# Kernel tuning notes

Hardware: AMD Instinct MI355X
Metric: run time of the kernel (lower is better)

Reference implementation:

```python
import jax, jax.numpy as jnp
import numpy as np

E = 256            # embedding_dim
S = 16             # num_surv_samples
N = 8192           # batch of events
NUM_NODES = 20000  # max_dst_idx - min_src_idx + 1
N_SRC = 10000
MIN_DST = 10000
TD_HR_MAX = 5000.0


def setup_inputs() -> dict:
    key = jax.random.key(0)
    ks = jax.random.split(key, 16)
    all_embeddings = jax.random.normal(ks[0], (NUM_NODES, E), dtype=jnp.float32)
    assoc = jnp.arange(NUM_NODES, dtype=jnp.int64 if jax.config.jax_enable_x64 else jnp.int32)
    src = jax.random.randint(ks[1], (N,), 0, N_SRC)
    pos_dst = jax.random.randint(ks[2], (N,), 0, N_SRC) + MIN_DST
    last_update = jax.random.uniform(ks[3], (NUM_NODES,), dtype=jnp.float32) * 1000.0
    last_time_pos = jax.random.uniform(ks[4], (N,), dtype=jnp.float32) * 1000.0
    cur_time = 2000.0 + jax.random.uniform(ks[5], (N,), dtype=jnp.float32) * 100.0
    u_non_embeddings = jax.random.normal(ks[6], (S * N, E), dtype=jnp.float32)
    v_non_embeddings = jax.random.normal(ks[7], (S * N, E), dtype=jnp.float32)
    td_surv_step = jax.random.uniform(ks[8], (S, N), dtype=jnp.float32)
    event_inten_accu = jax.random.uniform(ks[9], (N_SRC, N_SRC), dtype=jnp.float32)
    W_omega = jax.random.normal(ks[10], (1, 2 * E), dtype=jnp.float32) * (1.0 / np.sqrt(2 * E))
    b_omega = jax.random.normal(ks[11], (1,), dtype=jnp.float32) * 0.01
    psi = 0.5 * jnp.ones((1,), dtype=jnp.float32)
    alpha = jax.random.uniform(ks[12], (1,), dtype=jnp.float32)
    w_t = jax.random.uniform(ks[13], (1,), dtype=jnp.float32)
    return dict(all_embeddings=all_embeddings, assoc=assoc, src=src, pos_dst=pos_dst,
                last_update=last_update, cur_time=cur_time,
                u_non_embeddings=u_non_embeddings, v_non_embeddings=v_non_embeddings,
                last_time_pos=last_time_pos, td_surv_step=td_surv_step,
                event_inten_accu=event_inten_accu, W_omega=W_omega, b_omega=b_omega,
                psi=psi, alpha=alpha, w_t=w_t)


def _hawkes_intensity(z_u, z_v, td, W, b, psi, alpha, w_t):
    # symmetric=False path of hawkes_intensity_singleType
    Wu, Wv = W[0, :E], W[0, E:]          # split Linear over [z_u; z_v] concat
    g = z_u @ Wu + z_v @ Wv + b[0]       # [M]
    td_norm = td / TD_HR_MAX
    g = g + alpha[0] * jnp.exp(-w_t[0] * td_norm)
    g_psi = jnp.clip(g / (psi[0] + 1e-7), -75.0, 75.0)
    return psi[0] * (jnp.log1p(jnp.exp(-g_psi)) + g_psi)


def reference(all_embeddings, assoc, src, pos_dst, last_update, cur_time,
              u_non_embeddings, v_non_embeddings, last_time_pos, td_surv_step,
              event_inten_accu, W_omega, b_omega, psi, alpha, w_t):
    z_src = all_embeddings[assoc[src]]
    z_dst = all_embeddings[assoc[pos_dst]]
    lu_src = last_update[assoc[src]]
    lu_dst = last_update[assoc[pos_dst]]

    td_pos = cur_time - last_time_pos  # (unused downstream on this branch)
    last_update_max = jnp.maximum(lu_src, lu_dst)
    use_accu = (last_time_pos >= last_update_max).astype(jnp.float32)
    t_uv = jnp.maximum(last_update_max, last_time_pos)
    td_uv = cur_time - t_uv

    # unit_sampling=False: Monte-Carlo survival samples
    td_uv_non = td_surv_step * td_uv[None, :]          # [S, N]

    lambda_uv = _hawkes_intensity(z_src, z_dst, td_uv, W_omega, b_omega, psi, alpha, w_t)
    lambda_surv = _hawkes_intensity(u_non_embeddings, v_non_embeddings,
                                    td_uv_non.reshape(-1), W_omega, b_omega,
                                    psi, alpha, w_t).reshape(S, N)

    integral = jnp.mean(lambda_surv, axis=0) * td_uv \
        + use_accu * event_inten_accu[src, pos_dst - MIN_DST]
    loss_surv = jnp.sum(integral)
    loss_lambda = -jnp.sum(jnp.log(lambda_uv + 1e-7))

    n = z_src.shape[0]
    return (loss_lambda / n, loss_surv / n)
```

## Files before the change

kernel.cpp:

```cpp
#include <hip/hip_runtime.h>

constexpr int   S_    = 16;
constexpr int   N_    = 8192;
constexpr int   NSRC  = 10000;
constexpr int   MINDST= 10000;
constexpr float TDMAX = 5000.0f;

__device__ __forceinline__ float wave_reduce_sum(float v) {
#pragma unroll
    for (int off = 32; off > 0; off >>= 1)
        v += __shfl_xor(v, off, 64);
    return v;
}

__device__ __forceinline__ float hawkes(float gdot, float td,
                                        float b, float psi, float alpha, float wt) {
    float g  = gdot + b + alpha * expf(-wt * (td * (1.0f / TDMAX)));
    float gp = g / (psi + 1e-7f);
    gp = fminf(fmaxf(gp, -75.0f), 75.0f);
    return psi * (log1pf(expf(-gp)) + gp);
}

__global__ __launch_bounds__(256) void decoder_tp_fused(
    const float* __restrict__ emb,
    const int*   __restrict__ assoc,
    const int*   __restrict__ src,
    const int*   __restrict__ dst,
    const float* __restrict__ last_update,
    const float* __restrict__ cur_time,
    const float* __restrict__ u_non,
    const float* __restrict__ v_non,
    const float* __restrict__ last_time_pos,
    const float* __restrict__ td_step,
    const float* __restrict__ accu,
    const float* __restrict__ W,
    const float* __restrict__ b_p,
    const float* __restrict__ psi_p,
    const float* __restrict__ alpha_p,
    const float* __restrict__ wt_p,
    float* __restrict__ out)
{
    const int wave = threadIdx.x >> 6;
    const int lane = threadIdx.x & 63;
    const int i    = (blockIdx.x << 2) + wave;

    const float4* __restrict__ W4 = (const float4*)W;
    const float4 wu = W4[lane];
    const float4 wv = W4[64 + lane];
    const float b0    = b_p[0];
    const float psi   = psi_p[0];
    const float alpha = alpha_p[0];
    const float wt    = wt_p[0];

    const int si = src[i];
    const int di = dst[i];
    const int as = assoc[si];
    const int ad = assoc[di];
    const float lum  = fmaxf(last_update[as], last_update[ad]);
    const float ltp  = last_time_pos[i];
    const float ct   = cur_time[i];
    const float t_uv = fmaxf(lum, ltp);
    const float td_uv = ct - t_uv;

    const float4* __restrict__ Z4 = (const float4*)emb;
    const float4 zs = Z4[(size_t)as * 64 + lane];
    const float4 zd = Z4[(size_t)ad * 64 + lane];
    float d = zs.x * wu.x + zs.y * wu.y + zs.z * wu.z + zs.w * wu.w
            + zd.x * wv.x + zd.y * wv.y + zd.z * wv.z + zd.w * wv.w;
    d = wave_reduce_sum(d);
    const float lam_uv = hawkes(d, td_uv, b0, psi, alpha, wt);
    const float loss_lambda = -logf(lam_uv + 1e-7f);

    const float4* __restrict__ U4 = (const float4*)u_non;
    const float4* __restrict__ V4 = (const float4*)v_non;
    float lam_sum = 0.0f;
#pragma unroll 4
    for (int s = 0; s < S_; ++s) {
        const size_t p = (size_t)s * N_ + i;
        const float4 uu = U4[p * 64 + lane];
        const float4 vv = V4[p * 64 + lane];
        float dd = uu.x * wu.x + uu.y * wu.y + uu.z * wu.z + uu.w * wu.w
                 + vv.x * wv.x + vv.y * wv.y + vv.z * wv.z + vv.w * wv.w;
        dd = wave_reduce_sum(dd);
        lam_sum += hawkes(dd, td_step[p] * td_uv, b0, psi, alpha, wt);
    }
    float loss_surv = lam_sum * (1.0f / S_) * td_uv;
    if (ltp >= lum)
        loss_surv += accu[(size_t)si * NSRC + (di - MINDST)];

    __shared__ float s_ll[4], s_sv[4];
    if (lane == 0) { s_ll[wave] = loss_lambda; s_sv[wave] = loss_surv; }
    __syncthreads();
    if (threadIdx.x == 0) {
        const float a = s_ll[0] + s_ll[1] + s_ll[2] + s_ll[3];
        const float c = s_sv[0] + s_sv[1] + s_sv[2] + s_sv[3];
        atomicAdd(&out[0], a * (1.0f / N_));
        atomicAdd(&out[1], c * (1.0f / N_));
    }
}

extern "C" void kernel_launch(void* const* d_in, const int* in_sizes, int n_in,
                              void* d_out, int out_size, void* d_ws, size_t ws_size,
                              hipStream_t stream) {
    const float* emb           = (const float*)d_in[0];
    const int*   assoc         = (const int*)  d_in[1];
    const int*   src           = (const int*)  d_in[2];
    const int*   dst           = (const int*)  d_in[3];
    const float* last_update   = (const float*)d_in[4];
    const float* cur_time      = (const float*)d_in[5];
    const float* u_non         = (const float*)d_in[6];
    const float* v_non         = (const float*)d_in[7];
    const float* last_time_pos = (const float*)d_in[8];
    const float* td_step       = (const float*)d_in[9];
    const float* accu          = (const float*)d_in[10];
    const float* W             = (const float*)d_in[11];
    const float* b_p           = (const float*)d_in[12];
    const float* psi_p         = (const float*)d_in[13];
    const float* alpha_p       = (const float*)d_in[14];
    const float* wt_p          = (const float*)d_in[15];
    float* out = (float*)d_out;

    hipMemsetAsync(out, 0, 2 * sizeof(float), stream);

    decoder_tp_fused<<<N_ / 4, 256, 0, stream>>>(
        emb, assoc, src, dst, last_update, cur_time, u_non, v_non,
        last_time_pos, td_step, accu, W, b_p, psi_p, alpha_p, wt_p, out);
}
```

Measured before the change: 638.1 us.

## Split fused decoder into per-sample survival, lambda, and finalize kernels

The survival Monte-Carlo part now runs as its own kernel with one wave per (sample, event) pair, giving 16x more blocks instead of looping over 16 samples inside each wave. This is meant to expose more memory-level parallelism on the large u/v streams, which make up most of the traffic. The lambda and accu gathers move to a separate kernel. Global atomics are replaced by per-block partial sums in workspace plus a single-block finalize kernel, which removes the memset and atomics but adds two launches and recomputes td_uv per sample.

New measurement: 655.4 us. 2.7% more time.

```diff
diff --git a/kernel.cpp b/kernel.cpp
--- a/kernel.cpp
+++ b/kernel.cpp
@@ -1,10 +1,13 @@
 #include <hip/hip_runtime.h>
 
-constexpr int   S_    = 16;
-constexpr int   N_    = 8192;
-constexpr int   NSRC  = 10000;
-constexpr int   MINDST= 10000;
-constexpr float TDMAX = 5000.0f;
+constexpr int   S_     = 16;
+constexpr int   N_     = 8192;
+constexpr int   NSRC   = 10000;
+constexpr int   MINDST = 10000;
+constexpr float TDMAX  = 5000.0f;
+
+constexpr int SURV_BLOCKS = (S_ * N_) / 4;
+constexpr int LAM_BLOCKS  = N_ / 4;
 
 __device__ __forceinline__ float wave_reduce_sum(float v) {
 #pragma unroll
@@ -21,24 +24,79 @@
     return psi * (log1pf(expf(-gp)) + gp);
 }
 
-__global__ __launch_bounds__(256) void decoder_tp_fused(
+__global__ __launch_bounds__(256) void surv_kernel(
+    const int*   __restrict__ src,
+    const int*   __restrict__ dst,
+    const int*   __restrict__ assoc,
+    const float* __restrict__ last_update,
+    const float* __restrict__ cur_time,
+    const float* __restrict__ last_time_pos,
+    const float* __restrict__ u_non,
+    const float* __restrict__ v_non,
+    const float* __restrict__ td_step,
+    const float* __restrict__ W,
+    const float* __restrict__ b_p,
+    const float* __restrict__ psi_p,
+    const float* __restrict__ alpha_p,
+    const float* __restrict__ wt_p,
+    float* __restrict__ ws_s)
+{
+    const int wave = threadIdx.x >> 6;
+    const int lane = threadIdx.x & 63;
+    const int q    = (blockIdx.x << 2) + wave;
+    const int i    = q & (N_ - 1);
+
+    const float4* __restrict__ W4 = (const float4*)W;
+    const float4 wu = W4[lane];
+    const float4 wv = W4[64 + lane];
+
+    const float4* __restrict__ U4 = (const float4*)u_non;
+    const float4* __restrict__ V4 = (const float4*)v_non;
+    const float4 uu = U4[(size_t)q * 64 + lane];
+    const float4 vv = V4[(size_t)q * 64 + lane];
+    const float ts = td_step[q];
+
+    const int si = src[i];
+    const int di = dst[i];
+    const int as = assoc[si];
+    const int ad = assoc[di];
+    const float lum   = fmaxf(last_update[as], last_update[ad]);
+    const float td_uv = cur_time[i] - fmaxf(lum, last_time_pos[i]);
+
+    float d = uu.x * wu.x + uu.y * wu.y + uu.z * wu.z + uu.w * wu.w
+            + vv.x * wv.x + vv.y * wv.y + vv.z * wv.z + vv.w * wv.w;
+    d = wave_reduce_sum(d);
+
+    const float b0    = b_p[0];
+    const float psi   = psi_p[0];
+    const float alpha = alpha_p[0];
+    const float wt    = wt_p[0];
+    const float contrib = hawkes(d, ts * td_uv, b0, psi, alpha, wt)
+                        * td_uv * (1.0f / S_);
+
+    __shared__ float sh[4];
+    if (lane == 0) sh[wave] = contrib;
+    __syncthreads();
+    if (threadIdx.x == 0)
+        ws_s[blockIdx.x] = sh[0] + sh[1] + sh[2] + sh[3];
+}
+
+__global__ __launch_bounds__(256) void lambda_kernel(
     const float* __restrict__ emb,
     const int*   __restrict__ assoc,
     const int*   __restrict__ src,
     const int*   __restrict__ dst,
     const float* __restrict__ last_update,
     const float* __restrict__ cur_time,
-    const float* __restrict__ u_non,
-    const float* __restrict__ v_non,
     const float* __restrict__ last_time_pos,
-    const float* __restrict__ td_step,
     const float* __restrict__ accu,
     const float* __restrict__ W,
     const float* __restrict__ b_p,
     const float* __restrict__ psi_p,
     const float* __restrict__ alpha_p,
     const float* __restrict__ wt_p,
-    float* __restrict__ out)
+    float* __restrict__ ws_l,
+    float* __restrict__ ws_a)
 {
     const int wave = threadIdx.x >> 6;
     const int lane = threadIdx.x & 63;
@@ -47,20 +105,16 @@
     const float4* __restrict__ W4 = (const float4*)W;
     const float4 wu = W4[lane];
     const float4 wv = W4[64 + lane];
-    const float b0    = b_p[0];
-    const float psi   = psi_p[0];
-    const float alpha = alpha_p[0];
-    const float wt    = wt_p[0];
 
     const int si = src[i];
     const int di = dst[i];
     const int as = assoc[si];
     const int ad = assoc[di];
-    const float lum  = fmaxf(last_update[as], last_update[ad]);
-    const float ltp  = last_time_pos[i];
-    const float ct   = cur_time[i];
-    const float t_uv = fmaxf(lum, ltp);
-    const float td_uv = ct - t_uv;
+    const float lus = last_update[as];
+    const float lud = last_update[ad];
+    const float lum = fmaxf(lus, lud);
+    const float ltp = last_time_pos[i];
+    const float td_uv = cur_time[i] - fmaxf(lum, ltp);
 
     const float4* __restrict__ Z4 = (const float4*)emb;
     const float4 zs = Z4[(size_t)as * 64 + lane];
@@ -68,34 +122,45 @@
     float d = zs.x * wu.x + zs.y * wu.y + zs.z * wu.z + zs.w * wu.w
             + zd.x * wv.x + zd.y * wv.y + zd.z * wv.z + zd.w * wv.w;
     d = wave_reduce_sum(d);
-    const float lam_uv = hawkes(d, td_uv, b0, psi, alpha, wt);
-    const float loss_lambda = -logf(lam_uv + 1e-7f);
-
-    const float4* __restrict__ U4 = (const float4*)u_non;
-    const float4* __restrict__ V4 = (const float4*)v_non;
-    float lam_sum = 0.0f;
-#pragma unroll 4
-    for (int s = 0; s < S_; ++s) {
-        const size_t p = (size_t)s * N_ + i;
-        const float4 uu = U4[p * 64 + lane];
-        const float4 vv = V4[p * 64 + lane];
-        float dd = uu.x * wu.x + uu.y * wu.y + uu.z * wu.z + uu.w * wu.w
-                 + vv.x * wv.x + vv.y * wv.y + vv.z * wv.z + vv.w * wv.w;
-        dd = wave_reduce_sum(dd);
-        lam_sum += hawkes(dd, td_step[p] * td_uv, b0, psi, alpha, wt);
-    }
-    float loss_surv = lam_sum * (1.0f / S_) * td_uv;
-    if (ltp >= lum)
-        loss_surv += accu[(size_t)si * NSRC + (di - MINDST)];
-
-    __shared__ float s_ll[4], s_sv[4];
-    if (lane == 0) { s_ll[wave] = loss_lambda; s_sv[wave] = loss_surv; }
+
+    const float lam = hawkes(d, td_uv, b_p[0], psi_p[0], alpha_p[0], wt_p[0]);
+    const float part_l = -logf(lam + 1e-7f);
+
+    float part_a = accu[(size_t)si * NSRC + (di - MINDST)];
+    part_a = (ltp >= lum) ? part_a : 0.0f;
+
+    __shared__ float shl[4], sha[4];
+    if (lane == 0) { shl[wave] = part_l; sha[wave] = part_a; }
     __syncthreads();
     if (threadIdx.x == 0) {
-        const float a = s_ll[0] + s_ll[1] + s_ll[2] + s_ll[3];
-        const float c = s_sv[0] + s_sv[1] + s_sv[2] + s_sv[3];
-        atomicAdd(&out[0], a * (1.0f / N_));
-        atomicAdd(&out[1], c * (1.0f / N_));
+        ws_l[blockIdx.x] = shl[0] + shl[1] + shl[2] + shl[3];
+        ws_a[blockIdx.x] = sha[0] + sha[1] + sha[2] + sha[3];
+    }
+}
+
+__global__ __launch_bounds__(256) void finalize_kernel(
+    const float* __restrict__ ws_s,
+    const float* __restrict__ ws_l,
+    const float* __restrict__ ws_a,
+    float* __restrict__ out)
+{
+    float sS = 0.0f, sL = 0.0f;
+    for (int j = threadIdx.x; j < SURV_BLOCKS; j += 256) sS += ws_s[j];
+    for (int j = threadIdx.x; j < LAM_BLOCKS; j += 256) {
+        sS += ws_a[j];
+        sL += ws_l[j];
+    }
+    sS = wave_reduce_sum(sS);
+    sL = wave_reduce_sum(sL);
+
+    __shared__ float shS[4], shL[4];
+    const int wave = threadIdx.x >> 6;
+    const int lane = threadIdx.x & 63;
+    if (lane == 0) { shS[wave] = sS; shL[wave] = sL; }
+    __syncthreads();
+    if (threadIdx.x == 0) {
+        out[0] = (shL[0] + shL[1] + shL[2] + shL[3]) * (1.0f / N_);
+        out[1] = (shS[0] + shS[1] + shS[2] + shS[3]) * (1.0f / N_);
     }
 }
 
@@ -120,9 +185,17 @@
     const float* wt_p          = (const float*)d_in[15];
     float* out = (float*)d_out;
 
-    hipMemsetAsync(out, 0, 2 * sizeof(float), stream);
-
-    decoder_tp_fused<<<N_ / 4, 256, 0, stream>>>(
-        emb, assoc, src, dst, last_update, cur_time, u_non, v_non,
-        last_time_pos, td_step, accu, W, b_p, psi_p, alpha_p, wt_p, out);
-}
+    float* ws_s = (float*)d_ws;
+    float* ws_l = ws_s + SURV_BLOCKS;
+    float* ws_a = ws_l + LAM_BLOCKS;
+
+    surv_kernel<<<SURV_BLOCKS, 256, 0, stream>>>(
+        src, dst, assoc, last_update, cur_time, last_time_pos,
+        u_non, v_non, td_step, W, b_p, psi_p, alpha_p, wt_p, ws_s);
+
+    lambda_kernel<<<LAM_BLOCKS, 256, 0, stream>>>(
+        emb, assoc, src, dst, last_update, cur_time, last_time_pos,
+        accu, W, b_p, psi_p, alpha_p, wt_p, ws_l, ws_a);
+
+    finalize_kernel<<<1, 256, 0, stream>>>(ws_s, ws_l, ws_a, out);
+}
```

## Spread survival samples across waves and replace atomics with two-stage reduction

Applied to the files above, without the earlier changes.

Each wave now handles two survival samples (u/v rows) instead of one event's sixteen, so the grid grows from 2048 to 16384 blocks and all sample loads are issued up front for more memory-level parallelism. The per-event data (src/dst, last_update, td_uv) is recomputed by each wave that needs it, while the positive-pair intensity and accu term are computed only by the first N waves. Per-block partial sums go to workspace and a single-block finalize kernel reduces them, replacing the global atomics and the memset. This trades redundant per-event index and gather work and an extra launch for higher occupancy and streaming bandwidth on the dominant u/v read.

New measurement: 645.0 us. No clear change (+1.1%).

```diff
diff --git a/kernel.cpp b/kernel.cpp
--- a/kernel.cpp
+++ b/kernel.cpp
@@ -1,10 +1,13 @@
 #include <hip/hip_runtime.h>
 
-constexpr int   S_    = 16;
-constexpr int   N_    = 8192;
-constexpr int   NSRC  = 10000;
-constexpr int   MINDST= 10000;
-constexpr float TDMAX = 5000.0f;
+constexpr int   S_     = 16;
+constexpr int   N_     = 8192;
+constexpr int   NSRC   = 10000;
+constexpr int   MINDST = 10000;
+constexpr float TDMAX  = 5000.0f;
+
+constexpr int TOTAL_WAVES = S_ * N_ / 2;
+constexpr int MAIN_BLOCKS = TOTAL_WAVES / 4;
 
 __device__ __forceinline__ float wave_reduce_sum(float v) {
 #pragma unroll
@@ -21,16 +24,16 @@
     return psi * (log1pf(expf(-gp)) + gp);
 }
 
-__global__ __launch_bounds__(256) void decoder_tp_fused(
+__global__ __launch_bounds__(256) void fused_kernel(
     const float* __restrict__ emb,
     const int*   __restrict__ assoc,
     const int*   __restrict__ src,
     const int*   __restrict__ dst,
     const float* __restrict__ last_update,
     const float* __restrict__ cur_time,
+    const float* __restrict__ last_time_pos,
     const float* __restrict__ u_non,
     const float* __restrict__ v_non,
-    const float* __restrict__ last_time_pos,
     const float* __restrict__ td_step,
     const float* __restrict__ accu,
     const float* __restrict__ W,
@@ -38,64 +41,97 @@
     const float* __restrict__ psi_p,
     const float* __restrict__ alpha_p,
     const float* __restrict__ wt_p,
-    float* __restrict__ out)
+    float* __restrict__ ws_s,
+    float* __restrict__ ws_l)
 {
     const int wave = threadIdx.x >> 6;
     const int lane = threadIdx.x & 63;
-    const int i    = (blockIdx.x << 2) + wave;
+    const int w    = (blockIdx.x << 2) + wave;
+    const int q0   = w;
+    const int q1   = w + TOTAL_WAVES;
+    const int i    = w & (N_ - 1);
+
+    const float4* __restrict__ U4 = (const float4*)u_non;
+    const float4* __restrict__ V4 = (const float4*)v_non;
+    const float4 u0 = U4[(size_t)q0 * 64 + lane];
+    const float4 v0 = V4[(size_t)q0 * 64 + lane];
+    const float4 u1 = U4[(size_t)q1 * 64 + lane];
+    const float4 v1 = V4[(size_t)q1 * 64 + lane];
+    const float ts0 = td_step[q0];
+    const float ts1 = td_step[q1];
 
     const float4* __restrict__ W4 = (const float4*)W;
     const float4 wu = W4[lane];
     const float4 wv = W4[64 + lane];
+
+    const int si = src[i];
+    const int di = dst[i];
+    const int as = assoc[si];
+    const int ad = assoc[di];
+    const float lum   = fmaxf(last_update[as], last_update[ad]);
+    const float ltp   = last_time_pos[i];
+    const float td_uv = cur_time[i] - fmaxf(lum, ltp);
+
     const float b0    = b_p[0];
     const float psi   = psi_p[0];
     const float alpha = alpha_p[0];
     const float wt    = wt_p[0];
 
-    const int si = src[i];
-    const int di = dst[i];
-    const int as = assoc[si];
-    const int ad = assoc[di];
-    const float lum  = fmaxf(last_update[as], last_update[ad]);
-    const float ltp  = last_time_pos[i];
-    const float ct   = cur_time[i];
-    const float t_uv = fmaxf(lum, ltp);
-    const float td_uv = ct - t_uv;
+    float d0 = u0.x * wu.x + u0.y * wu.y + u0.z * wu.z + u0.w * wu.w
+             + v0.x * wv.x + v0.y * wv.y + v0.z * wv.z + v0.w * wv.w;
+    float d1 = u1.x * wu.x + u1.y * wu.y + u1.z * wu.z + u1.w * wu.w
+             + v1.x * wv.x + v1.y * wv.y + v1.z * wv.z + v1.w * wv.w;
+    d0 = wave_reduce_sum(d0);
+    d1 = wave_reduce_sum(d1);
 
-    const float4* __restrict__ Z4 = (const float4*)emb;
-    const float4 zs = Z4[(size_t)as * 64 + lane];
-    const float4 zd = Z4[(size_t)ad * 64 + lane];
-    float d = zs.x * wu.x + zs.y * wu.y + zs.z * wu.z + zs.w * wu.w
-            + zd.x * wv.x + zd.y * wv.y + zd.z * wv.z + zd.w * wv.w;
-    d = wave_reduce_sum(d);
-    const float lam_uv = hawkes(d, td_uv, b0, psi, alpha, wt);
-    const float loss_lambda = -logf(lam_uv + 1e-7f);
+    float contrib = (hawkes(d0, ts0 * td_uv, b0, psi, alpha, wt) +
+                     hawkes(d1, ts1 * td_uv, b0, psi, alpha, wt))
+                  * td_uv * (1.0f / S_);
+    float part_l = 0.0f;
 
-    const float4* __restrict__ U4 = (const float4*)u_non;
-    const float4* __restrict__ V4 = (const float4*)v_non;
-    float lam_sum = 0.0f;
-#pragma unroll 4
-    for (int s = 0; s < S_; ++s) {
-        const size_t p = (size_t)s * N_ + i;
-        const float4 uu = U4[p * 64 + lane];
-        const float4 vv = V4[p * 64 + lane];
-        float dd = uu.x * wu.x + uu.y * wu.y + uu.z * wu.z + uu.w * wu.w
-                 + vv.x * wv.x + vv.y * wv.y + vv.z * wv.z + vv.w * wv.w;
-        dd = wave_reduce_sum(dd);
-        lam_sum += hawkes(dd, td_step[p] * td_uv, b0, psi, alpha, wt);
+    if (w < N_) {
+        const float4* __restrict__ Z4 = (const float4*)emb;
+        const float4 zs = Z4[(size_t)as * 64 + lane];
+        const float4 zd = Z4[(size_t)ad * 64 + lane];
+        float d = zs.x * wu.x + zs.y * wu.y + zs.z * wu.z + zs.w * wu.w
+                + zd.x * wv.x + zd.y * wv.y + zd.z * wv.z + zd.w * wv.w;
+        d = wave_reduce_sum(d);
+        const float lam = hawkes(d, td_uv, b0, psi, alpha, wt);
+        part_l = -logf(lam + 1e-7f);
+        if (ltp >= lum)
+            contrib += accu[(size_t)si * NSRC + (di - MINDST)];
     }
-    float loss_surv = lam_sum * (1.0f / S_) * td_uv;
-    if (ltp >= lum)
-        loss_surv += accu[(size_t)si * NSRC + (di - MINDST)];
 
-    __shared__ float s_ll[4], s_sv[4];
-    if (lane == 0) { s_ll[wave] = loss_lambda; s_sv[wave] = loss_surv; }
+    __shared__ float sh_s[4], sh_l[4];
+    if (lane == 0) { sh_s[wave] = contrib; sh_l[wave] = part_l; }
     __syncthreads();
     if (threadIdx.x == 0) {
-        const float a = s_ll[0] + s_ll[1] + s_ll[2] + s_ll[3];
-        const float c = s_sv[0] + s_sv[1] + s_sv[2] + s_sv[3];
-        atomicAdd(&out[0], a * (1.0f / N_));
-        atomicAdd(&out[1], c * (1.0f / N_));
+        ws_s[blockIdx.x] = sh_s[0] + sh_s[1] + sh_s[2] + sh_s[3];
+        ws_l[blockIdx.x] = sh_l[0] + sh_l[1] + sh_l[2] + sh_l[3];
+    }
+}
+
+__global__ __launch_bounds__(256) void finalize_kernel(
+    const float* __restrict__ ws_s,
+    const float* __restrict__ ws_l,
+    float* __restrict__ out)
+{
+    float sS = 0.0f, sL = 0.0f;
+    for (int j = threadIdx.x; j < MAIN_BLOCKS; j += 256) {
+        sS += ws_s[j];
+        sL += ws_l[j];
+    }
+    sS = wave_reduce_sum(sS);
+    sL = wave_reduce_sum(sL);
+
+    __shared__ float shS[4], shL[4];
+    const int wave = threadIdx.x >> 6;
+    const int lane = threadIdx.x & 63;
+    if (lane == 0) { shS[wave] = sS; shL[wave] = sL; }
+    __syncthreads();
+    if (threadIdx.x == 0) {
+        out[0] = (shL[0] + shL[1] + shL[2] + shL[3]) * (1.0f / N_);
+        out[1] = (shS[0] + shS[1] + shS[2] + shS[3]) * (1.0f / N_);
     }
 }
 
@@ -120,9 +156,13 @@
     const float* wt_p          = (const float*)d_in[15];
     float* out = (float*)d_out;
 
-    hipMemsetAsync(out, 0, 2 * sizeof(float), stream);
+    float* ws_s = (float*)d_ws;
+    float* ws_l = ws_s + MAIN_BLOCKS;
 
-    decoder_tp_fused<<<N_ / 4, 256, 0, stream>>>(
-        emb, assoc, src, dst, last_update, cur_time, u_non, v_non,
-        last_time_pos, td_step, accu, W, b_p, psi_p, alpha_p, wt_p, out);
+    fused_kernel<<<MAIN_BLOCKS, 256, 0, stream>>>(
+        emb, assoc, src, dst, last_update, cur_time, last_time_pos,
+        u_non, v_non, td_step, accu, W, b_p, psi_p, alpha_p, wt_p,
+        ws_s, ws_l);
+
+    finalize_kernel<<<1, 256, 0, stream>>>(ws_s, ws_l, out);
 }
```
